# Kernel tuning notes

Hardware: AMD Instinct MI355X
Metric: run time of the kernel (lower is better)

The kernel has to match this reference:

```python
import jax, jax.numpy as jnp
import numpy as np

N_NODES = 100000
N_EDGES = 1600000
D_IN = 128
D_HID = 128
D_OUT = 128


def _sage_conv(x, src, dst, W_l, b_l, W_r, num_nodes):
    # PyG SAGEConv (aggr='mean'): out = lin_l(mean_{j in N(i)} x_j) + lin_r(x_i)
    msg = x[src]  # [E, d] gather source features
    agg = jax.ops.segment_sum(msg, dst, num_segments=num_nodes)  # [N, d]
    deg = jax.ops.segment_sum(jnp.ones((src.shape[0],), x.dtype), dst, num_segments=num_nodes)
    mean = agg / jnp.maximum(deg, 1.0)[:, None]
    return mean @ W_l.T + b_l + x @ W_r.T


def setup_inputs() -> dict:
    key = jax.random.key(0)
    ks = jax.random.split(key, 8)
    x = jax.random.normal(ks[0], (N_NODES, D_IN), dtype=jnp.float32)
    edge_index = jax.random.randint(ks[1], (2, N_EDGES), 0, N_NODES, dtype=jnp.int64)
    s = 1.0 / np.sqrt(D_IN)
    W_l1 = jax.random.uniform(ks[2], (D_HID, D_IN), jnp.float32, -s, s)
    b_l1 = jnp.zeros((D_HID,), jnp.float32)
    W_r1 = jax.random.uniform(ks[3], (D_HID, D_IN), jnp.float32, -s, s)
    s2 = 1.0 / np.sqrt(D_HID)
    W_l2 = jax.random.uniform(ks[4], (D_OUT, D_HID), jnp.float32, -s2, s2)
    b_l2 = jnp.zeros((D_OUT,), jnp.float32)
    W_r2 = jax.random.uniform(ks[5], (D_OUT, D_HID), jnp.float32, -s2, s2)
    return {"x": x, "edge_index": edge_index, "W_l1": W_l1, "b_l1": b_l1,
            "W_r1": W_r1, "W_l2": W_l2, "b_l2": b_l2, "W_r2": W_r2}


def reference(x, edge_index, W_l1, b_l1, W_r1, W_l2, b_l2, W_r2):
    src, dst = edge_index[0], edge_index[1]
    n = x.shape[0]
    h = _sage_conv(x, src, dst, W_l1, b_l1, W_r1, n)
    h = jax.nn.relu(h)
    out = _sage_conv(h, src, dst, W_l2, b_l2, W_r2, n)
    return out
```

## Files before the change

### kernel.cpp

```cpp
#include <hip/hip_runtime.h>
#include <stdint.h>

typedef short bf16x8 __attribute__((ext_vector_type(8)));
typedef unsigned short u16x8 __attribute__((ext_vector_type(8)));
typedef float f32x4 __attribute__((ext_vector_type(4)));

#define NPB 512
#define BSHIFT 9
#define MAXBUCK 256
#define STAGE_CAP 12288
#define LROW 136

__device__ __forceinline__ short f2bf(float f) {
    uint32_t u = __float_as_uint(f);
    u += 0x7fffu + ((u >> 16) & 1u);
    return (short)(u >> 16);
}
__device__ __forceinline__ float bf2f(unsigned short s) {
    return __uint_as_float((uint32_t)s << 16);
}

__global__ __launch_bounds__(256) void convx_kernel(const float* __restrict__ in,
                                                    short* __restrict__ out, int n) {
    int i = (blockIdx.x * 256 + threadIdx.x) * 8;
    if (i + 8 <= n) {
        const float4 v0 = *(const float4*)(in + i);
        const float4 v1 = *(const float4*)(in + i + 4);
        bf16x8 o;
        o[0] = f2bf(v0.x); o[1] = f2bf(v0.y); o[2] = f2bf(v0.z); o[3] = f2bf(v0.w);
        o[4] = f2bf(v1.x); o[5] = f2bf(v1.y); o[6] = f2bf(v1.z); o[7] = f2bf(v1.w);
        *(bf16x8*)(out + i) = o;
    } else {
        for (int j = i; j < n; ++j) out[j] = f2bf(in[j]);
    }
}

__global__ void convw4_kernel(const float* __restrict__ w0, const float* __restrict__ w1,
                              const float* __restrict__ w2, const float* __restrict__ w3,
                              short* __restrict__ o0, short* __restrict__ o1,
                              short* __restrict__ o2, short* __restrict__ o3) {
    int i = blockIdx.x * 256 + threadIdx.x;
    o0[i] = f2bf(w0[i]);
    o1[i] = f2bf(w1[i]);
    o2[i] = f2bf(w2[i]);
    o3[i] = f2bf(w3[i]);
}

__global__ __launch_bounds__(256) void bhist_kernel(const int* __restrict__ dst,
                                                    int* __restrict__ bcnt, int E, int B) {
    __shared__ int h[MAXBUCK];
    for (int i = threadIdx.x; i < B; i += 256) h[i] = 0;
    __syncthreads();
    int stride = gridDim.x * 256;
    for (int e = blockIdx.x * 256 + threadIdx.x; e < E; e += stride)
        atomicAdd(&h[dst[e] >> BSHIFT], 1);
    __syncthreads();
    for (int i = threadIdx.x; i < B; i += 256)
        if (h[i]) atomicAdd(&bcnt[i], h[i]);
}

__global__ __launch_bounds__(256) void bscan_kernel(const int* __restrict__ bcnt,
                                                    int* __restrict__ bbase,
                                                    int* __restrict__ gcur,
                                                    int* __restrict__ rowptr,
                                                    int E, int N, int B) {
    __shared__ int s[256];
    int t = threadIdx.x;
    int v = (t < B) ? bcnt[t] : 0;
    s[t] = v;
    __syncthreads();
    for (int off = 1; off < 256; off <<= 1) {
        int a = (t >= off) ? s[t - off] : 0;
        __syncthreads();
        s[t] += a;
        __syncthreads();
    }
    int excl = s[t] - v;
    if (t < B) { bbase[t] = excl; gcur[t] = excl; }
    if (t == B - 1) bbase[B] = excl + v;
    if (t == 0) rowptr[N] = E;
}

__global__ __launch_bounds__(256) void bin_kernel(const int* __restrict__ src,
                                                  const int* __restrict__ dst,
                                                  int* __restrict__ gcur,
                                                  unsigned int* __restrict__ binned,
                                                  int E, int B) {
    __shared__ int cnt[MAXBUCK];
    __shared__ int base[MAXBUCK];
    for (int i = threadIdx.x; i < B; i += 256) cnt[i] = 0;
    __syncthreads();
    const int e0 = blockIdx.x * 4096;
    const int eEnd = (e0 + 4096 < E) ? (e0 + 4096) : E;
#pragma unroll 4
    for (int e = e0 + threadIdx.x; e < eEnd; e += 256)
        atomicAdd(&cnt[dst[e] >> BSHIFT], 1);
    __syncthreads();
    for (int i = threadIdx.x; i < B; i += 256) {
        int c = cnt[i];
        base[i] = c ? atomicAdd(&gcur[i], c) : 0;
        cnt[i] = 0;
    }
    __syncthreads();
#pragma unroll 4
    for (int e = e0 + threadIdx.x; e < eEnd; e += 256) {
        int sv = src[e], dv = dst[e];
        int b = dv >> BSHIFT;
        int off = atomicAdd(&cnt[b], 1);
        binned[base[b] + off] = ((unsigned)sv << BSHIFT) | (unsigned)(dv & (NPB - 1));
    }
}

__global__ __launch_bounds__(256) void build_kernel(const unsigned int* __restrict__ binned,
                                                    const int* __restrict__ bbase,
                                                    int* __restrict__ rowptr,
                                                    int* __restrict__ csr, int N) {
    __shared__ int hist[NPB];
    __shared__ int cur[NPB];
    __shared__ int scanb[256];
    __shared__ int stage[STAGE_CAP];
    const int b = blockIdx.x;
    const int t = threadIdx.x;
    const int cbeg = bbase[b], cend = bbase[b + 1];
    const int cnt = cend - cbeg;
    for (int i = t; i < NPB; i += 256) hist[i] = 0;
    __syncthreads();
    for (int i = t; i < cnt; i += 256)
        atomicAdd(&hist[binned[cbeg + i] & (NPB - 1)], 1);
    __syncthreads();
    const int h0 = hist[2 * t], h1 = hist[2 * t + 1];
    const int ps = h0 + h1;
    scanb[t] = ps;
    __syncthreads();
    for (int off = 1; off < 256; off <<= 1) {
        int a = (t >= off) ? scanb[t - off] : 0;
        __syncthreads();
        scanb[t] += a;
        __syncthreads();
    }
    const int e0 = scanb[t] - ps;
    cur[2 * t]     = e0;
    cur[2 * t + 1] = e0 + h0;
    __syncthreads();
    const int node0 = b << BSHIFT;
    for (int i = t; i < NPB; i += 256) {
        int node = node0 + i;
        if (node < N) rowptr[node] = cbeg + cur[i];
    }
    __syncthreads();
    for (int i = t; i < cnt; i += 256) {
        unsigned rec = binned[cbeg + i];
        int ld  = rec & (NPB - 1);
        int pos = atomicAdd(&cur[ld], 1);
        if (pos < STAGE_CAP) stage[pos] = (int)(rec >> BSHIFT);
        else                 csr[cbeg + pos] = (int)(rec >> BSHIFT);
    }
    __syncthreads();
    const int lim = cnt < STAGE_CAP ? cnt : STAGE_CAP;
    for (int i = t; i < lim; i += 256)
        csr[cbeg + i] = stage[i];
}

#define ACC8(u) do { \
    a0 += bf2f(u[0]); a1 += bf2f(u[1]); a2 += bf2f(u[2]); a3 += bf2f(u[3]); \
    a4 += bf2f(u[4]); a5 += bf2f(u[5]); a6 += bf2f(u[6]); a7 += bf2f(u[7]); } while (0)

template <bool RELU>
__global__ __launch_bounds__(256) void fused_kernel(
    const short* __restrict__ feat, const int* __restrict__ csr,
    const int* __restrict__ rowptr,
    const short* __restrict__ Wl, const short* __restrict__ Wr,
    const float* __restrict__ bias,
    short* __restrict__ outb, float* __restrict__ outf, int N)
{
    __shared__ short lmean[64 * LROW];
    const int lane = threadIdx.x & 63;
    const int wave = threadIdx.x >> 6;
    const int q    = lane >> 4;
    const int ql   = lane & 15;
    const int m0   = blockIdx.x * 64 + wave * 16;

    for (int it = 0; it < 4; ++it) {
        const int node = m0 + it * 4 + q;
        float a0=0,a1=0,a2=0,a3=0,a4=0,a5=0,a6=0,a7=0;
        if (node < N) {
            const int beg = rowptr[node], end = rowptr[node + 1];
            int e = beg;
            for (; e + 8 <= end; e += 8) {
                const int s0 = csr[e],   s1 = csr[e+1], s2 = csr[e+2], s3 = csr[e+3];
                const int s4 = csr[e+4], s5 = csr[e+5], s6 = csr[e+6], s7 = csr[e+7];
                const u16x8 u0 = *(const u16x8*)(feat + (size_t)s0 * 128 + ql * 8);
                const u16x8 u1 = *(const u16x8*)(feat + (size_t)s1 * 128 + ql * 8);
                const u16x8 u2 = *(const u16x8*)(feat + (size_t)s2 * 128 + ql * 8);
                const u16x8 u3 = *(const u16x8*)(feat + (size_t)s3 * 128 + ql * 8);
                const u16x8 u4 = *(const u16x8*)(feat + (size_t)s4 * 128 + ql * 8);
                const u16x8 u5 = *(const u16x8*)(feat + (size_t)s5 * 128 + ql * 8);
                const u16x8 u6 = *(const u16x8*)(feat + (size_t)s6 * 128 + ql * 8);
                const u16x8 u7 = *(const u16x8*)(feat + (size_t)s7 * 128 + ql * 8);
                ACC8(u0); ACC8(u1); ACC8(u2); ACC8(u3);
                ACC8(u4); ACC8(u5); ACC8(u6); ACC8(u7);
            }
            if (e + 4 <= end) {
                const int s0 = csr[e], s1 = csr[e+1], s2 = csr[e+2], s3 = csr[e+3];
                const u16x8 u0 = *(const u16x8*)(feat + (size_t)s0 * 128 + ql * 8);
                const u16x8 u1 = *(const u16x8*)(feat + (size_t)s1 * 128 + ql * 8);
                const u16x8 u2 = *(const u16x8*)(feat + (size_t)s2 * 128 + ql * 8);
                const u16x8 u3 = *(const u16x8*)(feat + (size_t)s3 * 128 + ql * 8);
                ACC8(u0); ACC8(u1); ACC8(u2); ACC8(u3);
                e += 4;
            }
            for (; e < end; ++e) {
                const u16x8 u = *(const u16x8*)(feat + (size_t)csr[e] * 128 + ql * 8);
                ACC8(u);
            }
            const float r = 1.0f / fmaxf((float)(end - beg), 1.0f);
            bf16x8 o;
            o[0] = f2bf(a0 * r); o[1] = f2bf(a1 * r); o[2] = f2bf(a2 * r); o[3] = f2bf(a3 * r);
            o[4] = f2bf(a4 * r); o[5] = f2bf(a5 * r); o[6] = f2bf(a6 * r); o[7] = f2bf(a7 * r);
            *(bf16x8*)(lmean + (size_t)(wave * 16 + it * 4 + q) * LROW + ql * 8) = o;
        }
    }

    f32x4 acc[8];
#pragma unroll
    for (int i = 0; i < 8; ++i) acc[i] = (f32x4)0.0f;
    const bool valid = (m0 + ql < N);

#pragma unroll
    for (int kk = 0; kk < 4; ++kk) {
        const int kb = kk * 32 + q * 8;
        const bf16x8 a = *(const bf16x8*)(lmean + (size_t)(wave * 16 + ql) * LROW + kb);
#pragma unroll
        for (int nt = 0; nt < 8; ++nt) {
            const bf16x8 b = *(const bf16x8*)(Wl + (size_t)(nt * 16 + ql) * 128 + kb);
            acc[nt] = __builtin_amdgcn_mfma_f32_16x16x32_bf16(a, b, acc[nt], 0, 0, 0);
        }
    }
#pragma unroll
    for (int kk = 0; kk < 4; ++kk) {
        const int kb = kk * 32 + q * 8;
        bf16x8 a = (bf16x8)0;
        if (valid) a = *(const bf16x8*)(feat + (size_t)(m0 + ql) * 128 + kb);
#pragma unroll
        for (int nt = 0; nt < 8; ++nt) {
            const bf16x8 b = *(const bf16x8*)(Wr + (size_t)(nt * 16 + ql) * 128 + kb);
            acc[nt] = __builtin_amdgcn_mfma_f32_16x16x32_bf16(a, b, acc[nt], 0, 0, 0);
        }
    }

    const int rbase = m0 + q * 4;
#pragma unroll
    for (int nt = 0; nt < 8; ++nt) {
        const int col = nt * 16 + ql;
        const float bc = bias[col];
#pragma unroll
        for (int r = 0; r < 4; ++r) {
            const int node = rbase + r;
            if (node < N) {
                float v = acc[nt][r] + bc;
                if (RELU) outb[(size_t)node * 128 + col] = f2bf(fmaxf(v, 0.0f));
                else      outf[(size_t)node * 128 + col] = v;
            }
        }
    }
}

extern "C" void kernel_launch(void* const* d_in, const int* in_sizes, int n_in,
                              void* d_out, int out_size, void* d_ws, size_t ws_size,
                              hipStream_t stream) {
    const float* x   = (const float*)d_in[0];
    const int*   ei  = (const int*)d_in[1];
    const float* Wl1 = (const float*)d_in[2];
    const float* bl1 = (const float*)d_in[3];
    const float* Wr1 = (const float*)d_in[4];
    const float* Wl2 = (const float*)d_in[5];
    const float* bl2 = (const float*)d_in[6];
    const float* Wr2 = (const float*)d_in[7];

    const int N = in_sizes[0] / 128;
    const int E = in_sizes[1] / 2;
    const int* src = ei;
    const int* dst = ei + E;
    const int B = (N + NPB - 1) >> BSHIFT;

    char* wsb = (char*)d_ws;
    short* hbuf = (short*)wsb;
    size_t off = (size_t)N * 128 * 2;
    short* wl1 = (short*)(wsb + off); off += 16384 * 2;
    short* wr1 = (short*)(wsb + off); off += 16384 * 2;
    short* wl2 = (short*)(wsb + off); off += 16384 * 2;
    short* wr2 = (short*)(wsb + off); off += 16384 * 2;
    int* rowptr = (int*)(wsb + off);
    off += ((size_t)(N + 1) * 4 + 15) & ~(size_t)15;
    int* csr = (int*)(wsb + off);
    off += ((size_t)E * 4 + 15) & ~(size_t)15;
    unsigned int* binned = (unsigned int*)(wsb + off);
    off += ((size_t)E * 4 + 15) & ~(size_t)15;
    int* bcnt  = (int*)(wsb + off);
    int* bbase = bcnt + (MAXBUCK + 1);
    int* gcur  = bbase + (MAXBUCK + 1);

    short* xb  = (short*)d_out;
    float* out = (float*)d_out;

    const int fusedBlocks = (N + 63) / 64;
    const int binBlocks   = (E + 4095) / 4096;

    convx_kernel<<<(N * 128 / 8 + 255) / 256, 256, 0, stream>>>(x, xb, N * 128);
    convw4_kernel<<<64, 256, 0, stream>>>(Wl1, Wr1, Wl2, Wr2, wl1, wr1, wl2, wr2);

    (void)hipMemsetAsync(bcnt, 0, (size_t)(MAXBUCK + 1) * sizeof(int), stream);
    bhist_kernel<<<512, 256, 0, stream>>>(dst, bcnt, E, B);
    bscan_kernel<<<1, 256, 0, stream>>>(bcnt, bbase, gcur, rowptr, E, N, B);
    bin_kernel<<<binBlocks, 256, 0, stream>>>(src, dst, gcur, binned, E, B);
    build_kernel<<<B, 256, 0, stream>>>(binned, bbase, rowptr, csr, N);

    fused_kernel<true><<<fusedBlocks, 256, 0, stream>>>(xb, csr, rowptr, wl1, wr1, bl1,
                                                        hbuf, (float*)nullptr, N);
    fused_kernel<false><<<fusedBlocks, 256, 0, stream>>>(hbuf, csr, rowptr, wl2, wr2, bl2,
                                                         (short*)nullptr, out, N);
}
```

Before: 454.2 us.

## Halve nodes per block and split MFMA output columns across wave pairs

```diff
diff --git a/kernel.cpp b/kernel.cpp
--- a/kernel.cpp
+++ b/kernel.cpp
@@ -173,41 +173,28 @@
     const float* __restrict__ bias,
     short* __restrict__ outb, float* __restrict__ outf, int N)
 {
-    __shared__ short lmean[64 * LROW];
+    __shared__ short lmean[32 * LROW];
     const int lane = threadIdx.x & 63;
     const int wave = threadIdx.x >> 6;
     const int q    = lane >> 4;
     const int ql   = lane & 15;
-    const int m0   = blockIdx.x * 64 + wave * 16;
-
-    for (int it = 0; it < 4; ++it) {
-        const int node = m0 + it * 4 + q;
+    const int nb0  = blockIdx.x * 32;
+    const int m0w  = nb0 + wave * 8;
+
+    for (int it = 0; it < 2; ++it) {
+        const int node = m0w + it * 4 + q;
+        const int lrow = wave * 8 + it * 4 + q;
         float a0=0,a1=0,a2=0,a3=0,a4=0,a5=0,a6=0,a7=0;
         if (node < N) {
             const int beg = rowptr[node], end = rowptr[node + 1];
             int e = beg;
-            for (; e + 8 <= end; e += 8) {
-                const int s0 = csr[e],   s1 = csr[e+1], s2 = csr[e+2], s3 = csr[e+3];
-                const int s4 = csr[e+4], s5 = csr[e+5], s6 = csr[e+6], s7 = csr[e+7];
-                const u16x8 u0 = *(const u16x8*)(feat + (size_t)s0 * 128 + ql * 8);
-                const u16x8 u1 = *(const u16x8*)(feat + (size_t)s1 * 128 + ql * 8);
-                const u16x8 u2 = *(const u16x8*)(feat + (size_t)s2 * 128 + ql * 8);
-                const u16x8 u3 = *(const u16x8*)(feat + (size_t)s3 * 128 + ql * 8);
-                const u16x8 u4 = *(const u16x8*)(feat + (size_t)s4 * 128 + ql * 8);
-                const u16x8 u5 = *(const u16x8*)(feat + (size_t)s5 * 128 + ql * 8);
-                const u16x8 u6 = *(const u16x8*)(feat + (size_t)s6 * 128 + ql * 8);
-                const u16x8 u7 = *(const u16x8*)(feat + (size_t)s7 * 128 + ql * 8);
-                ACC8(u0); ACC8(u1); ACC8(u2); ACC8(u3);
-                ACC8(u4); ACC8(u5); ACC8(u6); ACC8(u7);
-            }
-            if (e + 4 <= end) {
+            for (; e + 4 <= end; e += 4) {
                 const int s0 = csr[e], s1 = csr[e+1], s2 = csr[e+2], s3 = csr[e+3];
                 const u16x8 u0 = *(const u16x8*)(feat + (size_t)s0 * 128 + ql * 8);
                 const u16x8 u1 = *(const u16x8*)(feat + (size_t)s1 * 128 + ql * 8);
                 const u16x8 u2 = *(const u16x8*)(feat + (size_t)s2 * 128 + ql * 8);
                 const u16x8 u3 = *(const u16x8*)(feat + (size_t)s3 * 128 + ql * 8);
                 ACC8(u0); ACC8(u1); ACC8(u2); ACC8(u3);
-                e += 4;
             }
             for (; e < end; ++e) {
                 const u16x8 u = *(const u16x8*)(feat + (size_t)csr[e] * 128 + ql * 8);
@@ -217,22 +204,28 @@
             bf16x8 o;
             o[0] = f2bf(a0 * r); o[1] = f2bf(a1 * r); o[2] = f2bf(a2 * r); o[3] = f2bf(a3 * r);
             o[4] = f2bf(a4 * r); o[5] = f2bf(a5 * r); o[6] = f2bf(a6 * r); o[7] = f2bf(a7 * r);
-            *(bf16x8*)(lmean + (size_t)(wave * 16 + it * 4 + q) * LROW + ql * 8) = o;
+            *(bf16x8*)(lmean + (size_t)lrow * LROW + ql * 8) = o;
+        } else {
+            *(bf16x8*)(lmean + (size_t)lrow * LROW + ql * 8) = (bf16x8)0;
         }
     }
-
-    f32x4 acc[8];
-#pragma unroll
-    for (int i = 0; i < 8; ++i) acc[i] = (f32x4)0.0f;
+    __syncthreads();
+
+    const int t2 = wave >> 1;
+    const int h  = wave & 1;
+    const int m0 = nb0 + t2 * 16;
+    f32x4 acc[4];
+#pragma unroll
+    for (int i = 0; i < 4; ++i) acc[i] = (f32x4)0.0f;
     const bool valid = (m0 + ql < N);
 
 #pragma unroll
     for (int kk = 0; kk < 4; ++kk) {
         const int kb = kk * 32 + q * 8;
-        const bf16x8 a = *(const bf16x8*)(lmean + (size_t)(wave * 16 + ql) * LROW + kb);
-#pragma unroll
-        for (int nt = 0; nt < 8; ++nt) {
-            const bf16x8 b = *(const bf16x8*)(Wl + (size_t)(nt * 16 + ql) * 128 + kb);
+        const bf16x8 a = *(const bf16x8*)(lmean + (size_t)(t2 * 16 + ql) * LROW + kb);
+#pragma unroll
+        for (int nt = 0; nt < 4; ++nt) {
+            const bf16x8 b = *(const bf16x8*)(Wl + (size_t)(h * 64 + nt * 16 + ql) * 128 + kb);
             acc[nt] = __builtin_amdgcn_mfma_f32_16x16x32_bf16(a, b, acc[nt], 0, 0, 0);
         }
     }
@@ -242,16 +235,16 @@
         bf16x8 a = (bf16x8)0;
         if (valid) a = *(const bf16x8*)(feat + (size_t)(m0 + ql) * 128 + kb);
 #pragma unroll
-        for (int nt = 0; nt < 8; ++nt) {
-            const bf16x8 b = *(const bf16x8*)(Wr + (size_t)(nt * 16 + ql) * 128 + kb);
+        for (int nt = 0; nt < 4; ++nt) {
+            const bf16x8 b = *(const bf16x8*)(Wr + (size_t)(h * 64 + nt * 16 + ql) * 128 + kb);
             acc[nt] = __builtin_amdgcn_mfma_f32_16x16x32_bf16(a, b, acc[nt], 0, 0, 0);
         }
     }
 
     const int rbase = m0 + q * 4;
 #pragma unroll
-    for (int nt = 0; nt < 8; ++nt) {
-        const int col = nt * 16 + ql;
+    for (int nt = 0; nt < 4; ++nt) {
+        const int col = h * 64 + nt * 16 + ql;
         const float bc = bias[col];
 #pragma unroll
         for (int r = 0; r < 4; ++r) {
@@ -303,7 +296,7 @@
     short* xb  = (short*)d_out;
     float* out = (float*)d_out;
 
-    const int fusedBlocks = (N + 63) / 64;
+    const int fusedBlocks = (N + 31) / 32;
     const int binBlocks   = (E + 4095) / 4096;
 
     convx_kernel<<<(N * 128 / 8 + 255) / 256, 256, 0, stream>>>(x, xb, N * 128);
```

After: 425.2 us. 6.4% less time.
